# Kernel tuning notes

Measured on AMD Instinct MI355X. Metric: run time of the kernel, lower is better.

The kernel has to match this reference:

```python
import jax, jax.numpy as jnp
import numpy as np

B, T_MEL, T_TXT = 16, 2048, 1024
D_MODEL, D_ENC_M, D_ENC_T = 512, 512, 512
LN_EPS = 1e-5


def setup_inputs() -> dict:
    key = jax.random.key(0)
    ks = jax.random.split(key, 9)
    mel_encoding = jax.random.normal(ks[0], (B, T_MEL, D_ENC_M), dtype=jnp.float32)
    text_encoding = jax.random.normal(ks[1], (B, T_TXT, D_ENC_T), dtype=jnp.float32)
    mel_mask = jax.random.randint(ks[2], (B, T_MEL), 0, 2).astype(bool)
    mel_mask = mel_mask.at[:, 0].set(False)  # guarantee >=1 unmasked key per row
    src_mask = jax.random.randint(ks[3], (B, T_TXT), 0, 2).astype(bool)
    # Projection weights stored [in, out] (torch Linear does x @ W.T)
    sc = 1.0 / np.sqrt(D_ENC_M)
    Wq = jax.random.uniform(ks[4], (D_ENC_T, D_MODEL), jnp.float32, -sc, sc)
    Wk = jax.random.uniform(ks[5], (D_ENC_M, D_MODEL), jnp.float32, -sc, sc)
    Wv = jax.random.uniform(ks[6], (D_ENC_M, D_MODEL), jnp.float32, -sc, sc)
    ln_gamma = jnp.ones((D_MODEL,), jnp.float32)
    ln_beta = jnp.zeros((D_MODEL,), jnp.float32)
    return {"mel_encoding": mel_encoding, "text_encoding": text_encoding,
            "mel_mask": mel_mask, "src_mask": src_mask,
            "Wq": Wq, "Wk": Wk, "Wv": Wv,
            "ln_gamma": ln_gamma, "ln_beta": ln_beta}


def reference(mel_encoding, text_encoding, mel_mask, src_mask, Wq, Wk, Wv, ln_gamma, ln_beta):
    temperature = jnp.sqrt(jnp.float32(D_ENC_M))
    q = jnp.einsum('btd,dm->btm', text_encoding, Wq)   # [B, T_txt, d_model]
    k = jnp.einsum('bsd,dm->bsm', mel_encoding, Wk)    # [B, T_mel, d_model]
    v = jnp.einsum('bsd,dm->bsm', mel_encoding, Wv)
    # attn_mask = outer product of src_mask and mel_mask (True -> masked)
    attn_mask = src_mask[:, :, None] & mel_mask[:, None, :]  # [B, T_txt, T_mel]
    scores = jnp.einsum('btm,bsm->bts', q, k) / temperature
    scores = jnp.where(attn_mask, -jnp.inf, scores)
    attn = jax.nn.softmax(scores, axis=2)
    output = jnp.einsum('bts,bsm->btm', attn, v)
    # dropout is identity at inference; LayerNorm over last dim
    mean = jnp.mean(output, axis=-1, keepdims=True)
    var = jnp.var(output, axis=-1, keepdims=True)
    output = (output - mean) * jax.lax.rsqrt(var + LN_EPS) * ln_gamma + ln_beta
    return output, attn
```

## Files before the change

### kernel.cpp

```cpp
#include <hip/hip_runtime.h>

#define DEV __device__ __forceinline__

typedef __attribute__((ext_vector_type(8))) short short8v;
typedef __attribute__((ext_vector_type(4))) float f32x4;

DEV unsigned short f2bf(float f) {
  unsigned int x = __float_as_uint(f);
  x = x + 0x7FFFu + ((x >> 16) & 1u);
  return (unsigned short)(x >> 16);
}
DEV float bf2f(unsigned short u) {
  return __uint_as_float(((unsigned)u) << 16);
}

DEV int swz_byte(int row, int kElem) {
  int chunk = ((kElem >> 3) ^ (row & 7));
  return row * 128 + (chunk << 4) + ((kElem & 7) << 1);
}

template <int ROUNDS>
DEV void stage(const unsigned short* __restrict__ g, int ld,
               unsigned short* tile, int tid) {
  const int wave = tid >> 6, l = tid & 63;
#pragma unroll
  for (int p = 0; p < ROUNDS; ++p) {
    const int r = (p << 5) + (wave << 3) + (l >> 3);
    const int c = ((l & 7) ^ (r & 7)) << 3;
    const unsigned short* src = g + (long)r * ld + c;
#if __has_builtin(__builtin_amdgcn_global_load_lds)
    unsigned short* dst = tile + (p << 11) + (wave << 9);
    __builtin_amdgcn_global_load_lds(
        (const __attribute__((address_space(1))) void*)src,
        (__attribute__((address_space(3))) void*)dst, 16, 0, 0);
#else
    short8v v = *reinterpret_cast<const short8v*>(src);
    *reinterpret_cast<short8v*>(reinterpret_cast<char*>(tile) +
                                (p << 12) + (wave << 10) + (l << 4)) = v;
#endif
  }
}

template <int BM>
DEV void stage_f32(const float* __restrict__ g, int ld,
                   unsigned short* tile, int tid) {
  const int rl = tid >> 4;
  const int c4 = (tid & 15) << 2;
#pragma unroll
  for (int p = 0; p < BM / 16; ++p) {
    const int row = (p << 4) + rl;
    const float4 f = *reinterpret_cast<const float4*>(g + (long)row * ld + c4);
    ushort4 pack;
    pack.x = f2bf(f.x); pack.y = f2bf(f.y); pack.z = f2bf(f.z); pack.w = f2bf(f.w);
    *reinterpret_cast<ushort4*>(reinterpret_cast<char*>(tile) +
                                swz_byte(row, c4)) = pack;
  }
}

template <int BM, int EPI, int GM, bool AF32>
__global__ __launch_bounds__(256) void gemm_bf16(
    const void* __restrict__ Av, const unsigned short* __restrict__ B,
    void* __restrict__ Cout, int M, int N, int K,
    long aBatch, long bBatch, long cBatch,
    const int* __restrict__ srcMask, const int* __restrict__ melMask,
    float scale, float* __restrict__ stats) {
  constexpr int NI = BM / 32;
  __shared__ unsigned short As[BM * 64];
  __shared__ unsigned short Bs[128 * 64];
  const int tid = threadIdx.x;
  const int lane = tid & 63;
  const int wave = tid >> 6;
  int z, bmi, bni;
  if constexpr (GM == 1) {
    const int id = blockIdx.x;
    z = (id & 7) | ((id >> 10) << 3);
    const int ib = (id >> 3) & 127;
    bni = ib & 15;
    bmi = ib >> 4;
  } else if constexpr (GM == 2) {
    bmi = blockIdx.x; bni = blockIdx.y; z = blockIdx.z;
  } else {
    bni = blockIdx.x; bmi = blockIdx.y; z = blockIdx.z;
  }
  const int bm = bmi * BM;
  const int bn = bni * 128;
  const unsigned short* Bb = B + (long)z * bBatch;
  const long cOff = (long)z * cBatch;
  const int wr = (wave >> 1) * (BM / 2);
  const int wc = (wave & 1) * 64;
  const int l15 = lane & 15;
  const int lHi = lane >> 4;

  f32x4 acc[NI][4] = {};

  for (int kt = 0; kt < K; kt += 64) {
    if constexpr (AF32) {
      stage_f32<BM>((const float*)Av + (long)z * aBatch + (long)bm * K + kt, K, As, tid);
    } else {
      stage<BM / 32>((const unsigned short*)Av + (long)z * aBatch + (long)bm * K + kt,
                     K, As, tid);
    }
    stage<4>(Bb + (long)bn * K + kt, K, Bs, tid);
    __syncthreads();
#pragma unroll
    for (int ks = 0; ks < 2; ++ks) {
      const int k0 = (ks << 5) + (lHi << 3);
      short8v af[NI], bfr[4];
#pragma unroll
      for (int i = 0; i < NI; ++i)
        af[i] = *reinterpret_cast<const short8v*>(
            reinterpret_cast<const char*>(As) + swz_byte(wr + i * 16 + l15, k0));
#pragma unroll
      for (int j = 0; j < 4; ++j)
        bfr[j] = *reinterpret_cast<const short8v*>(
            reinterpret_cast<const char*>(Bs) + swz_byte(wc + j * 16 + l15, k0));
#pragma unroll
      for (int i = 0; i < NI; ++i)
#pragma unroll
        for (int j = 0; j < 4; ++j)
          acc[i][j] = __builtin_amdgcn_mfma_f32_16x16x32_bf16(af[i], bfr[j], acc[i][j], 0, 0, 0);
    }
    __syncthreads();
  }

  if constexpr (EPI == 2) {
    __shared__ float redM[128][2];
    __shared__ float redS[128][2];
    const int wcIdx = wave & 1;
#pragma unroll
    for (int i = 0; i < NI; ++i) {
#pragma unroll
      for (int rr = 0; rr < 4; ++rr) {
        const int rloc = wr + i * 16 + lHi * 4 + rr;
        const int rb = bm + rloc;
        const bool sm = srcMask[z * 1024 + rb] != 0;
        float vals[4];
        float m_l = -3.0e38f;
#pragma unroll
        for (int j = 0; j < 4; ++j) {
          const int c = bn + wc + j * 16 + l15;
          const bool mm = melMask[z * 2048 + c] != 0;
          const float vf = (sm && mm) ? -1e30f : acc[i][j][rr] * scale;
          vals[j] = vf;
          reinterpret_cast<unsigned short*>(Cout)[cOff + (long)rb * N + c] = f2bf(vf);
          m_l = fmaxf(m_l, vf);
        }
#pragma unroll
        for (int o = 1; o < 16; o <<= 1) m_l = fmaxf(m_l, __shfl_xor(m_l, o, 64));
        float s_l = 0.f;
#pragma unroll
        for (int j = 0; j < 4; ++j) s_l += __expf(vals[j] - m_l);
#pragma unroll
        for (int o = 1; o < 16; o <<= 1) s_l += __shfl_xor(s_l, o, 64);
        if (l15 == 0) { redM[rloc][wcIdx] = m_l; redS[rloc][wcIdx] = s_l; }
      }
    }
    __syncthreads();
    if (tid < 128) {
      const float m0 = redM[tid][0], m1 = redM[tid][1];
      const float Mx = fmaxf(m0, m1);
      const float S = redS[tid][0] * __expf(m0 - Mx) + redS[tid][1] * __expf(m1 - Mx);
      const long sidx = ((long)(z * 1024 + bm + tid)) * 32 + (long)bni * 2;
      stats[sidx] = Mx;
      stats[sidx + 1] = S;
    }
  } else {
#pragma unroll
    for (int i = 0; i < NI; ++i) {
#pragma unroll
      for (int j = 0; j < 4; ++j) {
        const int rb = bm + wr + i * 16 + lHi * 4;
        const int c = bn + wc + j * 16 + l15;
#pragma unroll
        for (int r = 0; r < 4; ++r) {
          const long idx = cOff + (long)(rb + r) * N + c;
          reinterpret_cast<unsigned short*>(Cout)[idx] = f2bf(acc[i][j][r]);
        }
      }
    }
  }
}

__global__ __launch_bounds__(256) void pv_smx(
    const unsigned short* __restrict__ sbf, const unsigned short* __restrict__ vT,
    float* __restrict__ attn, float* __restrict__ out,
    const float* __restrict__ stats) {
  __shared__ unsigned short As[2][64 * 64];
  __shared__ unsigned short Bs[2][128 * 64];
  __shared__ float rowM[64], rowInv[64];
  const int id = blockIdx.x;
  const int z = (id & 7) | ((id >> 9) << 3);
  const int ib = (id >> 3) & 63;
  const int mt = ib & 15, nt = ib >> 4;
  const int bm = mt * 64, bn = nt * 128;
  const int tid = threadIdx.x, lane = tid & 63, wave = tid >> 6;

  if (tid < 64) {
    const float* st = stats + ((long)(z * 1024 + bm + tid)) * 32;
    float Mx = -3.0e38f;
#pragma unroll
    for (int t = 0; t < 16; ++t) Mx = fmaxf(Mx, st[t * 2]);
    float S = 0.f;
#pragma unroll
    for (int t = 0; t < 16; ++t) S += st[t * 2 + 1] * __expf(st[t * 2] - Mx);
    rowM[tid] = Mx;
    rowInv[tid] = 1.0f / S;
  }
  __syncthreads();

  const int ar = tid >> 2;
  const int ac = (tid & 3) << 4;
  const float mR = rowM[ar];
  const float invR = rowInv[ar];
  const long aOff = ((long)z * 1024 + bm + ar) * 2048 + ac;
  const unsigned short* vTb = vT + ((long)z * 512 + bn) * 2048;
  const int wr = (wave >> 1) * 32, wc = (wave & 1) * 64;
  const int l15 = lane & 15, lHi = lane >> 4;

  f32x4 acc[2][4] = {};

  for (int it = 0; it < 16; ++it) {
    const int kt = it << 7;
    stage<4>(vTb + kt, 2048, Bs[0], tid);
    stage<4>(vTb + kt + 64, 2048, Bs[1], tid);
#pragma unroll
    for (int h = 0; h < 2; ++h) {
      const int kh = kt + (h << 6);
      const short8v s0 = *reinterpret_cast<const short8v*>(sbf + aOff + kh);
      const short8v s1 = *reinterpret_cast<const short8v*>(sbf + aOff + kh + 8);
      float e[16];
#pragma unroll
      for (int u = 0; u < 8; ++u) {
        e[u] = __expf(bf2f((unsigned short)s0[u]) - mR) * invR;
        e[u + 8] = __expf(bf2f((unsigned short)s1[u]) - mR) * invR;
      }
      if ((kh >> 9) == nt) {
        float* ap = attn + aOff + kh;
#pragma unroll
        for (int g = 0; g < 4; ++g) {
          float4 w;
          w.x = e[g * 4]; w.y = e[g * 4 + 1]; w.z = e[g * 4 + 2]; w.w = e[g * 4 + 3];
          *reinterpret_cast<float4*>(ap + g * 4) = w;
        }
      }
      short8v pk0, pk1;
#pragma unroll
      for (int u = 0; u < 8; ++u) {
        pk0[u] = (short)f2bf(e[u]);
        pk1[u] = (short)f2bf(e[u + 8]);
      }
      *reinterpret_cast<short8v*>(reinterpret_cast<char*>(As[h]) + swz_byte(ar, ac)) = pk0;
      *reinterpret_cast<short8v*>(reinterpret_cast<char*>(As[h]) + swz_byte(ar, ac + 8)) = pk1;
    }
    __syncthreads();

#pragma unroll
    for (int h = 0; h < 2; ++h) {
#pragma unroll
      for (int ks = 0; ks < 2; ++ks) {
        const int k0 = (ks << 5) + (lHi << 3);
        short8v af[2], bfr[4];
#pragma unroll
        for (int i = 0; i < 2; ++i)
          af[i] = *reinterpret_cast<const short8v*>(
              reinterpret_cast<const char*>(As[h]) + swz_byte(wr + i * 16 + l15, k0));
#pragma unroll
        for (int j = 0; j < 4; ++j)
          bfr[j] = *reinterpret_cast<const short8v*>(
              reinterpret_cast<const char*>(Bs[h]) + swz_byte(wc + j * 16 + l15, k0));
#pragma unroll
        for (int i = 0; i < 2; ++i)
#pragma unroll
          for (int j = 0; j < 4; ++j)
            acc[i][j] = __builtin_amdgcn_mfma_f32_16x16x32_bf16(af[i], bfr[j], acc[i][j], 0, 0, 0);
      }
    }
    __syncthreads();
  }

#pragma unroll
  for (int i = 0; i < 2; ++i)
#pragma unroll
    for (int j = 0; j < 4; ++j) {
      const int row = bm + wr + i * 16 + lHi * 4;
      const int col = bn + wc + j * 16 + l15;
#pragma unroll
      for (int rr = 0; rr < 4; ++rr)
        out[((long)z * 1024 + row + rr) * 512 + col] = acc[i][j][rr];
    }
}

__global__ __launch_bounds__(256) void f32_to_bf16(
    const float* __restrict__ in, unsigned short* __restrict__ out, long n) {
  long i = ((long)blockIdx.x * blockDim.x + threadIdx.x) * 8;
  const long stride = (long)gridDim.x * blockDim.x * 8;
  for (; i < n; i += stride) {
    const float4 a = *reinterpret_cast<const float4*>(in + i);
    const float4 b = *reinterpret_cast<const float4*>(in + i + 4);
    short8v o;
    o[0] = (short)f2bf(a.x); o[1] = (short)f2bf(a.y);
    o[2] = (short)f2bf(a.z); o[3] = (short)f2bf(a.w);
    o[4] = (short)f2bf(b.x); o[5] = (short)f2bf(b.y);
    o[6] = (short)f2bf(b.z); o[7] = (short)f2bf(b.w);
    *reinterpret_cast<short8v*>(out + i) = o;
  }
}

__global__ __launch_bounds__(256) void prep_w(
    const float* __restrict__ Wq, const float* __restrict__ Wk,
    const float* __restrict__ Wv, unsigned short* __restrict__ wqbf,
    unsigned short* __restrict__ wkbf, unsigned short* __restrict__ WvT) {
  const int zz = blockIdx.z;
  const int tx = threadIdx.x, ty = threadIdx.y;
  if (zz == 0) {
    __shared__ float t[32][33];
    const int bx = blockIdx.x * 32;
    const int by = blockIdx.y * 32;
#pragma unroll
    for (int i = 0; i < 4; ++i)
      t[ty + i * 8][tx] = Wv[(long)(by + ty + i * 8) * 512 + bx + tx];
    __syncthreads();
#pragma unroll
    for (int i = 0; i < 4; ++i)
      WvT[(long)(bx + ty + i * 8) * 512 + by + tx] = f2bf(t[tx][ty + i * 8]);
  } else {
    const float* in = (zz == 1) ? Wq : Wk;
    unsigned short* out = (zz == 1) ? wqbf : wkbf;
    const long base = ((long)(blockIdx.y * 16 + blockIdx.x) * 256 + ty * 32 + tx) * 4;
    const float4 f = *reinterpret_cast<const float4*>(in + base);
    ushort4 o;
    o.x = f2bf(f.x); o.y = f2bf(f.y); o.z = f2bf(f.z); o.w = f2bf(f.w);
    *reinterpret_cast<ushort4*>(out + base) = o;
  }
}

__global__ __launch_bounds__(64) void layernorm_rows(
    float* __restrict__ out, const float* __restrict__ gamma, const float* __restrict__ beta) {
  const long row = blockIdx.x;
  float4* p = reinterpret_cast<float4*>(out + row * 512);
  const int lane = threadIdx.x;
  float4 a = p[lane];
  float4 b = p[lane + 64];
  float s = ((a.x + a.y) + (a.z + a.w)) + ((b.x + b.y) + (b.z + b.w));
  float s2 = ((a.x * a.x + a.y * a.y) + (a.z * a.z + a.w * a.w)) +
             ((b.x * b.x + b.y * b.y) + (b.z * b.z + b.w * b.w));
#pragma unroll
  for (int o = 32; o; o >>= 1) {
    s += __shfl_xor(s, o, 64);
    s2 += __shfl_xor(s2, o, 64);
  }
  const float mean = s * (1.0f / 512.0f);
  const float var = s2 * (1.0f / 512.0f) - mean * mean;
  const float rstd = rsqrtf(var + 1e-5f);
  const float4 g0 = reinterpret_cast<const float4*>(gamma)[lane];
  const float4 g1 = reinterpret_cast<const float4*>(gamma)[lane + 64];
  const float4 c0 = reinterpret_cast<const float4*>(beta)[lane];
  const float4 c1 = reinterpret_cast<const float4*>(beta)[lane + 64];
  a.x = (a.x - mean) * rstd * g0.x + c0.x;
  a.y = (a.y - mean) * rstd * g0.y + c0.y;
  a.z = (a.z - mean) * rstd * g0.z + c0.z;
  a.w = (a.w - mean) * rstd * g0.w + c0.w;
  b.x = (b.x - mean) * rstd * g1.x + c1.x;
  b.y = (b.y - mean) * rstd * g1.y + c1.y;
  b.z = (b.z - mean) * rstd * g1.z + c1.z;
  b.w = (b.w - mean) * rstd * g1.w + c1.w;
  p[lane] = a;
  p[lane + 64] = b;
}

extern "C" void kernel_launch(void* const* d_in, const int* in_sizes, int n_in,
                              void* d_out, int out_size, void* d_ws, size_t ws_size,
                              hipStream_t stream) {
  const float* mel  = (const float*)d_in[0];
  const float* text = (const float*)d_in[1];
  const int* melMask = (const int*)d_in[2];
  const int* srcMask = (const int*)d_in[3];
  const float* Wq = (const float*)d_in[4];
  const float* Wk = (const float*)d_in[5];
  const float* Wv = (const float*)d_in[6];
  const float* gamma = (const float*)d_in[7];
  const float* beta  = (const float*)d_in[8];

  float* out = (float*)d_out;
  float* attn = (float*)d_out + (long)16 * 1024 * 512;

  unsigned short* ws = (unsigned short*)d_ws;
  unsigned short* wqbf = ws;
  unsigned short* wkbf = wqbf + 512 * 512;
  unsigned short* wvT  = wkbf + 512 * 512;
  unsigned short* Mt   = wvT + 512 * 512;
  unsigned short* melbf = Mt + 512 * 512;
  unsigned short* qbf  = melbf + (long)16 * 2048 * 512;
  unsigned short* vT   = qbf + (long)16 * 1024 * 512;
  unsigned short* sbf  = vT + (long)16 * 512 * 2048;
  float* stats = (float*)(sbf + (long)16 * 1024 * 2048);

  prep_w<<<dim3(16, 16, 3), dim3(32, 8), 0, stream>>>(Wq, Wk, Wv, wqbf, wkbf, wvT);
  f32_to_bf16<<<dim3(4096), 256, 0, stream>>>(mel, melbf, (long)16 * 2048 * 512);

  gemm_bf16<128, 0, 0, false><<<dim3(4, 4, 1), 256, 0, stream>>>(
      wkbf, wqbf, Mt, 512, 512, 512, 0, 0, 0, nullptr, nullptr, 1.0f, nullptr);
  gemm_bf16<128, 0, 2, true><<<dim3(128, 4, 1), 256, 0, stream>>>(
      text, Mt, qbf, 16384, 512, 512, 0, 0, 0, nullptr, nullptr, 1.0f, nullptr);
  gemm_bf16<128, 0, 0, false><<<dim3(16, 4, 16), 256, 0, stream>>>(
      wvT, melbf, vT, 512, 2048, 512, 0, (long)2048 * 512, (long)512 * 2048,
      nullptr, nullptr, 1.0f, nullptr);
  gemm_bf16<128, 2, 1, false><<<dim3(2048), 256, 0, stream>>>(
      qbf, melbf, sbf, 1024, 2048, 512,
      (long)1024 * 512, (long)2048 * 512, (long)1024 * 2048,
      srcMask, melMask, 0.044194173824159216f, stats);
  pv_smx<<<dim3(1024), 256, 0, stream>>>(sbf, vT, attn, out, stats);
  layernorm_rows<<<dim3(16 * 1024), 64, 0, stream>>>(out, gamma, beta);
}
```

Before: 261.0 us.

## Load PV operands directly into MFMA registers, dropping LDS staging

```diff
diff --git a/kernel.cpp b/kernel.cpp
--- a/kernel.cpp
+++ b/kernel.cpp
@@ -181,12 +181,10 @@
   }
 }
 
-__global__ __launch_bounds__(256) void pv_smx(
+__global__ __launch_bounds__(256) void pv_reg(
     const unsigned short* __restrict__ sbf, const unsigned short* __restrict__ vT,
     float* __restrict__ attn, float* __restrict__ out,
     const float* __restrict__ stats) {
-  __shared__ unsigned short As[2][64 * 64];
-  __shared__ unsigned short Bs[2][128 * 64];
   __shared__ float rowM[64], rowInv[64];
   const int id = blockIdx.x;
   const int z = (id & 7) | ((id >> 9) << 3);
@@ -208,74 +206,60 @@
   }
   __syncthreads();
 
-  const int ar = tid >> 2;
-  const int ac = (tid & 3) << 4;
-  const float mR = rowM[ar];
-  const float invR = rowInv[ar];
-  const long aOff = ((long)z * 1024 + bm + ar) * 2048 + ac;
-  const unsigned short* vTb = vT + ((long)z * 512 + bn) * 2048;
   const int wr = (wave >> 1) * 32, wc = (wave & 1) * 64;
   const int l15 = lane & 15, lHi = lane >> 4;
+  const int r0 = wr + l15, r1 = wr + 16 + l15;
+  const float m0 = rowM[r0], v0 = rowInv[r0];
+  const float m1 = rowM[r1], v1 = rowInv[r1];
+  const int k8 = lHi << 3;
+  const unsigned short* a0 = sbf + ((long)(z * 1024 + bm + r0)) * 2048 + k8;
+  const unsigned short* a1 = sbf + ((long)(z * 1024 + bm + r1)) * 2048 + k8;
+  const unsigned short* b0 =
+      vT + ((long)(z * 512 + bn + wc + l15)) * 2048 + k8;
+  float* at0 = attn + ((long)(z * 1024 + bm + r0)) * 2048 + k8;
+  float* at1 = attn + ((long)(z * 1024 + bm + r1)) * 2048 + k8;
+  const bool ownA = (wave & 1) == 0;
+  const int ktlo = nt << 9, kthi = (nt + 1) << 9;
 
   f32x4 acc[2][4] = {};
 
-  for (int it = 0; it < 16; ++it) {
-    const int kt = it << 7;
-    stage<4>(vTb + kt, 2048, Bs[0], tid);
-    stage<4>(vTb + kt + 64, 2048, Bs[1], tid);
-#pragma unroll
-    for (int h = 0; h < 2; ++h) {
-      const int kh = kt + (h << 6);
-      const short8v s0 = *reinterpret_cast<const short8v*>(sbf + aOff + kh);
-      const short8v s1 = *reinterpret_cast<const short8v*>(sbf + aOff + kh + 8);
-      float e[16];
-#pragma unroll
-      for (int u = 0; u < 8; ++u) {
-        e[u] = __expf(bf2f((unsigned short)s0[u]) - mR) * invR;
-        e[u + 8] = __expf(bf2f((unsigned short)s1[u]) - mR) * invR;
-      }
-      if ((kh >> 9) == nt) {
-        float* ap = attn + aOff + kh;
-#pragma unroll
-        for (int g = 0; g < 4; ++g) {
-          float4 w;
-          w.x = e[g * 4]; w.y = e[g * 4 + 1]; w.z = e[g * 4 + 2]; w.w = e[g * 4 + 3];
-          *reinterpret_cast<float4*>(ap + g * 4) = w;
-        }
-      }
-      short8v pk0, pk1;
-#pragma unroll
-      for (int u = 0; u < 8; ++u) {
-        pk0[u] = (short)f2bf(e[u]);
-        pk1[u] = (short)f2bf(e[u + 8]);
-      }
-      *reinterpret_cast<short8v*>(reinterpret_cast<char*>(As[h]) + swz_byte(ar, ac)) = pk0;
-      *reinterpret_cast<short8v*>(reinterpret_cast<char*>(As[h]) + swz_byte(ar, ac + 8)) = pk1;
-    }
-    __syncthreads();
-
-#pragma unroll
-    for (int h = 0; h < 2; ++h) {
-#pragma unroll
-      for (int ks = 0; ks < 2; ++ks) {
-        const int k0 = (ks << 5) + (lHi << 3);
-        short8v af[2], bfr[4];
-#pragma unroll
-        for (int i = 0; i < 2; ++i)
-          af[i] = *reinterpret_cast<const short8v*>(
-              reinterpret_cast<const char*>(As[h]) + swz_byte(wr + i * 16 + l15, k0));
-#pragma unroll
-        for (int j = 0; j < 4; ++j)
-          bfr[j] = *reinterpret_cast<const short8v*>(
-              reinterpret_cast<const char*>(Bs[h]) + swz_byte(wc + j * 16 + l15, k0));
-#pragma unroll
-        for (int i = 0; i < 2; ++i)
-#pragma unroll
-          for (int j = 0; j < 4; ++j)
-            acc[i][j] = __builtin_amdgcn_mfma_f32_16x16x32_bf16(af[i], bfr[j], acc[i][j], 0, 0, 0);
-      }
-    }
-    __syncthreads();
+#pragma unroll 2
+  for (int kt = 0; kt < 2048; kt += 32) {
+    const short8v sa0 = *reinterpret_cast<const short8v*>(a0 + kt);
+    const short8v sa1 = *reinterpret_cast<const short8v*>(a1 + kt);
+    short8v bfr[4];
+#pragma unroll
+    for (int j = 0; j < 4; ++j)
+      bfr[j] = *reinterpret_cast<const short8v*>(b0 + (long)j * 16 * 2048 + kt);
+
+    float e0[8], e1[8];
+#pragma unroll
+    for (int u = 0; u < 8; ++u) {
+      e0[u] = __expf(bf2f((unsigned short)sa0[u]) - m0) * v0;
+      e1[u] = __expf(bf2f((unsigned short)sa1[u]) - m1) * v1;
+    }
+    if (ownA && kt >= ktlo && kt < kthi) {
+      float4 w;
+      w.x = e0[0]; w.y = e0[1]; w.z = e0[2]; w.w = e0[3];
+      *reinterpret_cast<float4*>(at0 + kt) = w;
+      w.x = e0[4]; w.y = e0[5]; w.z = e0[6]; w.w = e0[7];
+      *reinterpret_cast<float4*>(at0 + kt + 4) = w;
+      w.x = e1[0]; w.y = e1[1]; w.z = e1[2]; w.w = e1[3];
+      *reinterpret_cast<float4*>(at1 + kt) = w;
+      w.x = e1[4]; w.y = e1[5]; w.z = e1[6]; w.w = e1[7];
+      *reinterpret_cast<float4*>(at1 + kt + 4) = w;
+    }
+    short8v p0, p1;
+#pragma unroll
+    for (int u = 0; u < 8; ++u) {
+      p0[u] = (short)f2bf(e0[u]);
+      p1[u] = (short)f2bf(e1[u]);
+    }
+#pragma unroll
+    for (int j = 0; j < 4; ++j) {
+      acc[0][j] = __builtin_amdgcn_mfma_f32_16x16x32_bf16(p0, bfr[j], acc[0][j], 0, 0, 0);
+      acc[1][j] = __builtin_amdgcn_mfma_f32_16x16x32_bf16(p1, bfr[j], acc[1][j], 0, 0, 0);
+    }
   }
 
 #pragma unroll
@@ -409,6 +393,6 @@
       qbf, melbf, sbf, 1024, 2048, 512,
       (long)1024 * 512, (long)2048 * 512, (long)1024 * 2048,
       srcMask, melMask, 0.044194173824159216f, stats);
-  pv_smx<<<dim3(1024), 256, 0, stream>>>(sbf, vT, attn, out, stats);
+  pv_reg<<<dim3(1024), 256, 0, stream>>>(sbf, vT, attn, out, stats);
   layernorm_rows<<<dim3(16 * 1024), 64, 0, stream>>>(out, gamma, beta);
 }
```

Measured after the change: 348.7 us. +33.6%, slower.

## Store locally-normalized exponentials in score kernel and rescale per chunk in PV kernel

Applied to the files above, without the earlier changes.

```diff
diff --git a/kernel.cpp b/kernel.cpp
--- a/kernel.cpp
+++ b/kernel.cpp
@@ -124,8 +124,6 @@
   }
 
   if constexpr (EPI == 2) {
-    __shared__ float redM[128][2];
-    __shared__ float redS[128][2];
     const int wcIdx = wave & 1;
 #pragma unroll
     for (int i = 0; i < NI; ++i) {
@@ -142,27 +140,26 @@
           const bool mm = melMask[z * 2048 + c] != 0;
           const float vf = (sm && mm) ? -1e30f : acc[i][j][rr] * scale;
           vals[j] = vf;
-          reinterpret_cast<unsigned short*>(Cout)[cOff + (long)rb * N + c] = f2bf(vf);
           m_l = fmaxf(m_l, vf);
         }
 #pragma unroll
         for (int o = 1; o < 16; o <<= 1) m_l = fmaxf(m_l, __shfl_xor(m_l, o, 64));
         float s_l = 0.f;
 #pragma unroll
-        for (int j = 0; j < 4; ++j) s_l += __expf(vals[j] - m_l);
+        for (int j = 0; j < 4; ++j) {
+          const float pe = __expf(vals[j] - m_l);
+          s_l += pe;
+          const int c = bn + wc + j * 16 + l15;
+          reinterpret_cast<unsigned short*>(Cout)[cOff + (long)rb * N + c] = f2bf(pe);
+        }
 #pragma unroll
         for (int o = 1; o < 16; o <<= 1) s_l += __shfl_xor(s_l, o, 64);
-        if (l15 == 0) { redM[rloc][wcIdx] = m_l; redS[rloc][wcIdx] = s_l; }
-      }
-    }
-    __syncthreads();
-    if (tid < 128) {
-      const float m0 = redM[tid][0], m1 = redM[tid][1];
-      const float Mx = fmaxf(m0, m1);
-      const float S = redS[tid][0] * __expf(m0 - Mx) + redS[tid][1] * __expf(m1 - Mx);
-      const long sidx = ((long)(z * 1024 + bm + tid)) * 32 + (long)bni * 2;
-      stats[sidx] = Mx;
-      stats[sidx + 1] = S;
+        if (l15 == 0) {
+          const long sidx = ((long)(z * 1024 + rb)) * 64 + (long)(bni * 2 + wcIdx) * 2;
+          stats[sidx] = m_l;
+          stats[sidx + 1] = s_l;
+        }
+      }
     }
   } else {
 #pragma unroll
@@ -187,7 +184,7 @@
     const float* __restrict__ stats) {
   __shared__ unsigned short As[2][64 * 64];
   __shared__ unsigned short Bs[2][128 * 64];
-  __shared__ float rowM[64], rowInv[64];
+  __shared__ unsigned short scl[64][32];
   const int id = blockIdx.x;
   const int z = (id & 7) | ((id >> 9) << 3);
   const int ib = (id >> 3) & 63;
@@ -195,23 +192,25 @@
   const int bm = mt * 64, bn = nt * 128;
   const int tid = threadIdx.x, lane = tid & 63, wave = tid >> 6;
 
-  if (tid < 64) {
-    const float* st = stats + ((long)(z * 1024 + bm + tid)) * 32;
+  {
+    const int row = tid >> 2;
+    const float* st = stats + ((long)(z * 1024 + bm + row)) * 64;
     float Mx = -3.0e38f;
 #pragma unroll
-    for (int t = 0; t < 16; ++t) Mx = fmaxf(Mx, st[t * 2]);
+    for (int t = 0; t < 32; ++t) Mx = fmaxf(Mx, st[t * 2]);
     float S = 0.f;
 #pragma unroll
-    for (int t = 0; t < 16; ++t) S += st[t * 2 + 1] * __expf(st[t * 2] - Mx);
-    rowM[tid] = Mx;
-    rowInv[tid] = 1.0f / S;
+    for (int t = 0; t < 32; ++t) S += st[t * 2 + 1] * __expf(st[t * 2] - Mx);
+    const float inv = 1.0f / S;
+    const int t0 = (tid & 3) * 8;
+#pragma unroll
+    for (int t = 0; t < 8; ++t)
+      scl[row][t0 + t] = f2bf(__expf(st[(t0 + t) * 2] - Mx) * inv);
   }
   __syncthreads();
 
   const int ar = tid >> 2;
   const int ac = (tid & 3) << 4;
-  const float mR = rowM[ar];
-  const float invR = rowInv[ar];
   const long aOff = ((long)z * 1024 + bm + ar) * 2048 + ac;
   const unsigned short* vTb = vT + ((long)z * 512 + bn) * 2048;
   const int wr = (wave >> 1) * 32, wc = (wave & 1) * 64;
@@ -226,13 +225,14 @@
 #pragma unroll
     for (int h = 0; h < 2; ++h) {
       const int kh = kt + (h << 6);
+      const float sc = bf2f(scl[ar][kh >> 6]);
       const short8v s0 = *reinterpret_cast<const short8v*>(sbf + aOff + kh);
       const short8v s1 = *reinterpret_cast<const short8v*>(sbf + aOff + kh + 8);
       float e[16];
 #pragma unroll
       for (int u = 0; u < 8; ++u) {
-        e[u] = __expf(bf2f((unsigned short)s0[u]) - mR) * invR;
-        e[u + 8] = __expf(bf2f((unsigned short)s1[u]) - mR) * invR;
+        e[u] = bf2f((unsigned short)s0[u]) * sc;
+        e[u + 8] = bf2f((unsigned short)s1[u]) * sc;
       }
       if ((kh >> 9) == nt) {
         float* ap = attn + aOff + kh;
```

After: 259.3 us. About the same (-0.7%).
